# Kernel optimization log

Measured on AMD Instinct MI355X. Metric: run time of the kernel, lower is better.

Reference implementation:

```python
import jax, jax.numpy as jnp
import numpy as np
from jax import lax

N, H, W, CIN = 64, 256, 256, 3   # batch, image HxW, RGB
C, K = 32, 5                     # cross-conv channels / kernel size (from reshape(-1,32,5,5))
ADIM, AHID = 4, 256              # action dim, action-encoder hidden


def _conv(x, w, b, stride, pad):
    # x [N,C,H,W], w [O,I,kh,kw] (torch OIHW cross-correlation semantics)
    y = lax.conv_general_dilated(x, w, (stride, stride), [(pad, pad), (pad, pad)],
                                 dimension_numbers=('NCHW', 'OIHW', 'NCHW'))
    return y + b[None, :, None, None]


def cross_convolve(feat, kernels):
    # feat [N,C,h,w], kernels [N,C,K,K]; per-sample per-channel 'same' conv (padding=2).
    # Equivalent to the original N*C loop of tiny F.conv2d calls: one depthwise
    # (grouped, feature_group_count=C) conv per sample, vmapped over the batch.
    def one(x, k):  # x [C,h,w], k [C,K,K]
        y = lax.conv_general_dilated(x[None], k[:, None], (1, 1), [(2, 2), (2, 2)],
                                     dimension_numbers=('NCHW', 'OIHW', 'NCHW'),
                                     feature_group_count=C)
        return y[0]
    return jax.vmap(one)(feat, kernels)


def setup_inputs() -> dict:
    key = jax.random.key(0)
    ks = jax.random.split(key, 10)
    g = lambda i, shape, s: jax.random.normal(ks[i], shape, jnp.float32) * s
    return {
        'images': jax.random.normal(ks[0], (N, H, W, CIN), jnp.float32),
        'actions': jax.random.normal(ks[1], (N, ADIM), jnp.float32),
        # phys_encoder: conv(3->32,k5,s2,p2) relu, conv(32->32,k5,s2,p2) relu
        'pe_w1': g(2, (C, CIN, 5, 5), 0.08), 'pe_b1': jnp.zeros((C,), jnp.float32),
        'pe_w2': g(3, (C, C, 5, 5), 0.04), 'pe_b2': jnp.zeros((C,), jnp.float32),
        # action_encoder MLP: ADIM -> AHID -> C*K*K (=800)
        'ae_w1': g(4, (ADIM, AHID), 0.3), 'ae_b1': jnp.zeros((AHID,), jnp.float32),
        'ae_w2': g(5, (AHID, C * K * K), 0.05), 'ae_b2': jnp.zeros((C * K * K,), jnp.float32),
        # motion_predictor: conv(32->32,k3,p1) relu, conv(32->2,k3,p1)
        'mp_w1': g(6, (C, C, 3, 3), 0.06), 'mp_b1': jnp.zeros((C,), jnp.float32),
        'mp_w2': g(7, (2, C, 3, 3), 0.06), 'mp_b2': jnp.zeros((2,), jnp.float32),
    }


def reference(images, actions, pe_w1, pe_b1, pe_w2, pe_b2,
              ae_w1, ae_b1, ae_w2, ae_b2, mp_w1, mp_b1, mp_w2, mp_b2):
    x = jnp.transpose(images, (0, 3, 1, 2))                 # NHWC -> NCHW
    h = jax.nn.relu(_conv(x, pe_w1, pe_b1, 2, 2))           # [N,32,128,128]
    h = jax.nn.relu(_conv(h, pe_w2, pe_b2, 2, 2))           # [N,32,64,64]
    a = jax.nn.relu(actions @ ae_w1 + ae_b1)
    a = (a @ ae_w2 + ae_b2).reshape(-1, C, K, K)            # per-sample kernels [N,32,5,5]
    sa = cross_convolve(h, a)                               # [N,32,64,64]
    f = jax.nn.relu(_conv(sa, mp_w1, mp_b1, 1, 1))
    flow = _conv(f, mp_w2, mp_b2, 1, 1)                     # [N,2,64,64]
    return flow
```

## Files before the change

kernel.cpp:

```cpp
#include <hip/hip_runtime.h>


typedef __attribute__((ext_vector_type(8))) short bf16x8;
typedef __attribute__((ext_vector_type(4))) float f32x4;
typedef __attribute__((ext_vector_type(16))) float f32x16;

__device__ __forceinline__ unsigned short f2bf(float f) {
    unsigned int u = __float_as_uint(f);
    u = (u + 0x7FFFu + ((u >> 16) & 1u)) >> 16;
    return (unsigned short)u;
}
__device__ __forceinline__ float bf2f(unsigned short h) {
    return __uint_as_float(((unsigned int)h) << 16);
}

__global__ __launch_bounds__(64) void zero_border_kernel(unsigned int* t, int R, int pad) {
    int row = blockIdx.x % R;
    int n   = blockIdx.x / R;
    int tid = threadIdx.x;
    unsigned int* rp = t + (size_t)(n * R + row) * R * 16;
    if (row < pad || row >= R - pad) {
        for (int i = tid; i < R * 16; i += 64) rp[i] = 0u;
    } else {
        for (int i = tid; i < pad * 16; i += 64) {
            rp[i] = 0u;
            rp[(size_t)(R - pad) * 16 + i] = 0u;
        }
    }
}

__global__ __launch_bounds__(256) void pad_img_kernel(const float* __restrict__ img,
                                                      unsigned short* __restrict__ imgp) {
    const int py = blockIdx.x % 260;
    const int n  = blockIdx.x / 260;
    const int iy = py - 2;
    const bool rowok = (iy >= 0) && (iy < 256);
    const float* srow = img + ((size_t)n * 256 + (rowok ? iy : 0)) * 768;
    unsigned short* drow = imgp + (size_t)(n * 260 + py) * 1056;
    for (int s = threadIdx.x; s < 1056; s += 256) {
        int px = s >> 2, c = s & 3;
        int ix = px - 2;
        float v = 0.f;
        if (rowok && c < 3 && ix >= 0 && ix < 256) v = srow[ix * 3 + c];
        drow[s] = f2bf(v);
    }
}

__global__ __launch_bounds__(256) void repack_conv1b(const float* __restrict__ src, unsigned short* __restrict__ dst) {
    int idx = blockIdx.x * 256 + threadIdx.x;
    if (idx >= 5120) return;
    int kh = idx / 1024, r = idx % 1024, o = r / 32, k = r % 32, dx = k >> 2, c = k & 3;
    float v = (dx < 5 && c < 3) ? src[o * 75 + c * 25 + kh * 5 + dx] : 0.f;
    dst[idx] = f2bf(v);
}
__global__ __launch_bounds__(256) void repack_conv2(const float* __restrict__ src, unsigned short* __restrict__ dst) {
    int idx = blockIdx.x * 256 + threadIdx.x;
    if (idx >= 25600) return;
    int co = idx / 800, r = idx % 800, ci = r / 25, tap = r % 25;
    dst[(tap * 32 + co) * 32 + ci] = f2bf(src[idx]);
}
__global__ __launch_bounds__(256) void repack_mp1(const float* __restrict__ src, unsigned short* __restrict__ dst) {
    int idx = blockIdx.x * 256 + threadIdx.x;
    if (idx >= 9216) return;
    int co = idx / 288, r = idx % 288, ci = r / 9, tap = r % 9;
    dst[(tap * 32 + co) * 32 + ci] = f2bf(src[idx]);
}
__global__ __launch_bounds__(256) void repack_mp2b(const float* __restrict__ src, unsigned short* __restrict__ dst) {
    int idx = blockIdx.x * 256 + threadIdx.x;
    if (idx >= 4608) return;
    int tap = idx / 512, r = idx % 512, co = r / 32, ci = r % 32;
    float v = (co < 2) ? src[co * 288 + ci * 9 + tap] : 0.f;
    dst[idx] = f2bf(v);
}

__global__ __launch_bounds__(256) void mlp_kernel(const float* __restrict__ actions,
                                                  const float* __restrict__ w1,
                                                  const float* __restrict__ b1,
                                                  const float* __restrict__ w2,
                                                  const float* __restrict__ b2,
                                                  float* __restrict__ aout) {
    int n = blockIdx.y;
    int t = threadIdx.x;
    __shared__ float hid[256];
    float a0 = actions[n * 4 + 0], a1 = actions[n * 4 + 1];
    float a2 = actions[n * 4 + 2], a3 = actions[n * 4 + 3];
    float acc = b1[t];
    acc += a0 * w1[0 * 256 + t] + a1 * w1[1 * 256 + t] +
           a2 * w1[2 * 256 + t] + a3 * w1[3 * 256 + t];
    hid[t] = fmaxf(acc, 0.0f);
    __syncthreads();
    int o = blockIdx.x * 200 + t;
    if (t < 200) {
        float s = b2[o];
        #pragma unroll 4
        for (int i = 0; i < 256; ++i) s += hid[i] * w2[i * 800 + o];
        aout[n * 800 + o] = s;
    }
}

__global__ __launch_bounds__(256) void conv1_mfma(const unsigned short* __restrict__ imgp,
                                                  const short* __restrict__ B1,
                                                  const float* __restrict__ bias,
                                                  unsigned short* __restrict__ h1p) {
    const int tid = threadIdx.x;
    const int lane = tid & 63;
    const int w = tid >> 6;
    const int n = blockIdx.y;
    const int cohalf = w & 1;
    const int oy = blockIdx.x * 2 + (w >> 1);
    const int ml = lane & 15;
    const int kg = lane >> 4;

    bf16x8 bfrag[5];
    #pragma unroll
    for (int kh = 0; kh < 5; ++kh)
        bfrag[kh] = *(const bf16x8*)(B1 + ((kh * 32 + cohalf * 16 + ml) * 32 + kg * 8));
    const float bia = bias[cohalf * 16 + ml];
    const int co = cohalf * 16 + ml;

    f32x4 acc[8];
    #pragma unroll
    for (int t = 0; t < 8; ++t) acc[t] = (f32x4){bia, bia, bia, bia};

    #pragma unroll
    for (int kh = 0; kh < 5; ++kh) {
        const unsigned short* rowbase = imgp + (size_t)(n * 260 + 2 * oy + kh) * 1056;
        #pragma unroll
        for (int t = 0; t < 8; ++t) {
            const int px0 = 2 * (16 * t + ml) + 2 * kg;
            bf16x8 af = *(const bf16x8*)(rowbase + px0 * 4);
            acc[t] = __builtin_amdgcn_mfma_f32_16x16x32_bf16(af, bfrag[kh], acc[t], 0, 0, 0);
        }
    }
    #pragma unroll
    for (int t = 0; t < 8; ++t) {
        #pragma unroll
        for (int r = 0; r < 4; ++r) {
            const int px = 16 * t + kg * 4 + r;
            h1p[((size_t)(n * 132 + oy + 2) * 132 + px + 2) * 32 + co] = f2bf(fmaxf(acc[t][r], 0.f));
        }
    }
}

__global__ __launch_bounds__(256, 6) void conv2_mfma32(const unsigned short* __restrict__ h1p,
                                                       const unsigned int* __restrict__ B,
                                                       const float* __restrict__ bias,
                                                       unsigned short* __restrict__ h2p) {
    __shared__ unsigned int Bs[5 * 32 * 20];
    const int tid = threadIdx.x;
    const int lane = tid & 63;
    const int w = tid >> 6;
    const int n = blockIdx.y;
    const int oy = blockIdx.x * 2 + (w >> 1);
    const int x0 = (w & 1) * 32;
    const int co = lane & 31;
    const int kgrp = lane >> 5;

    const float bia = bias[co];
    f32x16 acc;
    #pragma unroll
    for (int r = 0; r < 16; ++r) acc[r] = bia;

    const unsigned short* bbase = (const unsigned short*)Bs + co * 40 + kgrp * 8;
    const int px0 = 2 * (x0 + co);

    for (int kh = 0; kh < 5; ++kh) {
        if (kh) __syncthreads();
        const unsigned int* src = B + kh * 2560;
        #pragma unroll
        for (int i = tid; i < 2560; i += 256) {
            int row = i >> 4, p = i & 15;
            Bs[row * 20 + p] = src[i];
        }
        __syncthreads();

        const unsigned short* rowbase = h1p + (size_t)(n * 132 + 2 * oy + kh) * (132 * 32) + kgrp * 8;
        #pragma unroll
        for (int kw = 0; kw < 5; ++kw) {
            bf16x8 a0 = *(const bf16x8*)(rowbase + (px0 + kw) * 32);
            bf16x8 a1 = *(const bf16x8*)(rowbase + (px0 + kw) * 32 + 16);
            bf16x8 b0 = *(const bf16x8*)(bbase + kw * (32 * 40));
            bf16x8 b1 = *(const bf16x8*)(bbase + kw * (32 * 40) + 16);
            acc = __builtin_amdgcn_mfma_f32_32x32x16_bf16(a0, b0, acc, 0, 0, 0);
            acc = __builtin_amdgcn_mfma_f32_32x32x16_bf16(a1, b1, acc, 0, 0, 0);
        }
    }
    #pragma unroll
    for (int r = 0; r < 16; ++r) {
        const int px = (r & 3) + 8 * (r >> 2) + 4 * kgrp;
        const int ox = x0 + px;
        h2p[((size_t)(n * 68 + oy + 2) * 68 + ox + 2) * 32 + co] = f2bf(fmaxf(acc[r], 0.f));
    }
}

__global__ __launch_bounds__(256) void xconv_kernel(const unsigned short* __restrict__ h2p,
                                                    const float* __restrict__ ker,
                                                    unsigned short* __restrict__ sap) {
    __shared__ __align__(16) unsigned short tile[12 * 68 * 32];
    const int tid = threadIdx.x;
    const int n = blockIdx.x;
    const int rb = blockIdx.y;
    const unsigned short* src = h2p + (size_t)(n * 68 + rb * 8) * (68 * 32);
    for (int i = tid; i < 3264; i += 256)
        *(uint4*)(tile + i * 8) = *(const uint4*)(src + i * 8);
    const int ci = tid & 31, xg = tid >> 5;
    const float* kp = ker + (size_t)(n * 32 + ci) * 25;
    float k[25];
    #pragma unroll
    for (int t = 0; t < 25; ++t) k[t] = kp[t];
    __syncthreads();

    float acc[8][8];
    #pragma unroll
    for (int r = 0; r < 8; ++r)
        #pragma unroll
        for (int j = 0; j < 8; ++j) acc[r][j] = 0.f;

    #pragma unroll
    for (int ir = 0; ir < 12; ++ir) {
        float v[12];
        #pragma unroll
        for (int t = 0; t < 12; ++t)
            v[t] = bf2f(tile[(ir * 68 + xg * 8 + t) * 32 + ci]);
        #pragma unroll
        for (int kh = 0; kh < 5; ++kh) {
            const int r = ir - kh;
            if (r >= 0 && r < 8) {
                #pragma unroll
                for (int j = 0; j < 8; ++j) {
                    float s = acc[r][j];
                    #pragma unroll
                    for (int kw = 0; kw < 5; ++kw) s += k[kh * 5 + kw] * v[j + kw];
                    acc[r][j] = s;
                }
            }
        }
    }
    #pragma unroll
    for (int r = 0; r < 8; ++r)
        #pragma unroll
        for (int j = 0; j < 8; ++j)
            sap[((size_t)(n * 66 + rb * 8 + r + 1) * 66 + xg * 8 + j + 1) * 32 + ci] = f2bf(acc[r][j]);
}

__global__ __launch_bounds__(256, 6) void mp1_mfma32(const unsigned short* __restrict__ sap,
                                                     const unsigned int* __restrict__ B,
                                                     const float* __restrict__ bias,
                                                     unsigned short* __restrict__ fp) {
    __shared__ unsigned int Bs[9 * 32 * 20];
    const int tid = threadIdx.x;
    #pragma unroll
    for (int i = tid; i < 4608; i += 256) {
        int row = i >> 4, p = i & 15;
        Bs[row * 20 + p] = B[i];
    }
    __syncthreads();

    const int lane = tid & 63;
    const int w = tid >> 6;
    const int n = blockIdx.y;
    const int oy = blockIdx.x * 2 + (w >> 1);
    const int x0 = (w & 1) * 32;
    const int co = lane & 31;
    const int kgrp = lane >> 5;

    const float bia = bias[co];
    f32x16 acc;
    #pragma unroll
    for (int r = 0; r < 16; ++r) acc[r] = bia;

    const unsigned short* bbase = (const unsigned short*)Bs + co * 40 + kgrp * 8;
    const int px0 = x0 + co;

    #pragma unroll
    for (int kh = 0; kh < 3; ++kh) {
        const unsigned short* rowbase = sap + (size_t)(n * 66 + oy + kh) * (66 * 32) + kgrp * 8;
        #pragma unroll
        for (int kw = 0; kw < 3; ++kw) {
            const int tap = kh * 3 + kw;
            bf16x8 a0 = *(const bf16x8*)(rowbase + (px0 + kw) * 32);
            bf16x8 a1 = *(const bf16x8*)(rowbase + (px0 + kw) * 32 + 16);
            bf16x8 b0 = *(const bf16x8*)(bbase + tap * (32 * 40));
            bf16x8 b1 = *(const bf16x8*)(bbase + tap * (32 * 40) + 16);
            acc = __builtin_amdgcn_mfma_f32_32x32x16_bf16(a0, b0, acc, 0, 0, 0);
            acc = __builtin_amdgcn_mfma_f32_32x32x16_bf16(a1, b1, acc, 0, 0, 0);
        }
    }
    #pragma unroll
    for (int r = 0; r < 16; ++r) {
        const int px = (r & 3) + 8 * (r >> 2) + 4 * kgrp;
        const int ox = x0 + px;
        fp[((size_t)(n * 66 + oy + 1) * 66 + ox + 1) * 32 + co] = f2bf(fmaxf(acc[r], 0.f));
    }
}

__global__ __launch_bounds__(256) void mp2_mfma(const unsigned short* __restrict__ fpb,
                                                const short* __restrict__ B,
                                                const float* __restrict__ bias,
                                                float* __restrict__ out) {
    const int tid = threadIdx.x;
    const int lane = tid & 63;
    const int w = tid >> 6;
    const int n = blockIdx.y;
    const int oy = blockIdx.x * 4 + w;
    const int ml = lane & 15;
    const int kg = lane >> 4;

    bf16x8 bfrag[9];
    #pragma unroll
    for (int t = 0; t < 9; ++t)
        bfrag[t] = *(const bf16x8*)(B + ((t * 16 + ml) * 32 + kg * 8));
    const float bia = (ml < 2) ? bias[ml] : 0.f;

    f32x4 acc[4];
    #pragma unroll
    for (int t = 0; t < 4; ++t) acc[t] = (f32x4){bia, bia, bia, bia};

    #pragma unroll
    for (int kh = 0; kh < 3; ++kh) {
        const unsigned short* rowbase = fpb + (size_t)(n * 66 + oy + kh) * (66 * 32);
        #pragma unroll
        for (int kw = 0; kw < 3; ++kw) {
            #pragma unroll
            for (int t = 0; t < 4; ++t) {
                bf16x8 af = *(const bf16x8*)(rowbase + (16 * t + ml + kw) * 32 + kg * 8);
                acc[t] = __builtin_amdgcn_mfma_f32_16x16x32_bf16(af, bfrag[kh * 3 + kw], acc[t], 0, 0, 0);
            }
        }
    }
    if (ml < 2) {
        #pragma unroll
        for (int t = 0; t < 4; ++t) {
            #pragma unroll
            for (int r = 0; r < 4; ++r) {
                const int px = 16 * t + kg * 4 + r;
                out[(size_t)n * 8192 + (size_t)ml * 4096 + (size_t)oy * 64 + px] = acc[t][r];
            }
        }
    }
}

extern "C" void kernel_launch(void* const* d_in, const int* in_sizes, int n_in,
                              void* d_out, int out_size, void* d_ws, size_t ws_size,
                              hipStream_t stream) {
    (void)in_sizes; (void)n_in; (void)out_size; (void)ws_size;
    const float* images  = (const float*)d_in[0];
    const float* actions = (const float*)d_in[1];
    const float* pe_w1   = (const float*)d_in[2];
    const float* pe_b1   = (const float*)d_in[3];
    const float* pe_w2   = (const float*)d_in[4];
    const float* pe_b2   = (const float*)d_in[5];
    const float* ae_w1   = (const float*)d_in[6];
    const float* ae_b1   = (const float*)d_in[7];
    const float* ae_w2   = (const float*)d_in[8];
    const float* ae_b2   = (const float*)d_in[9];
    const float* mp_w1   = (const float*)d_in[10];
    const float* mp_b1   = (const float*)d_in[11];
    const float* mp_w2   = (const float*)d_in[12];
    const float* mp_b2   = (const float*)d_in[13];
    float* out = (float*)d_out;

    char* ws = (char*)d_ws;
    float* a_ker          = (float*)(ws + 0);
    unsigned short* B1    = (unsigned short*)(ws + 204800);
    unsigned short* B2    = (unsigned short*)(ws + 215040);
    unsigned short* Bm1   = (unsigned short*)(ws + 266240);
    unsigned short* Bm2   = (unsigned short*)(ws + 284672);
    unsigned short* h1p   = (unsigned short*)(ws + 524288);
    unsigned short* imgp  = (unsigned short*)(ws + 71892992);
    unsigned short* h2p   = (unsigned short*)(ws + 71892992);
    unsigned short* sap   = (unsigned short*)(ws + 90832896);
    unsigned short* fpb   = (unsigned short*)(ws + 108675072);

    repack_conv1b<<<20, 256, 0, stream>>>(pe_w1, B1);
    repack_conv2<<<100, 256, 0, stream>>>(pe_w2, B2);
    repack_mp1<<<36, 256, 0, stream>>>(mp_w1, Bm1);
    repack_mp2b<<<18, 256, 0, stream>>>(mp_w2, Bm2);
    mlp_kernel<<<dim3(4, 64), 256, 0, stream>>>(actions, ae_w1, ae_b1, ae_w2, ae_b2, a_ker);

    zero_border_kernel<<<64 * 132, 64, 0, stream>>>((unsigned int*)h1p, 132, 2);
    zero_border_kernel<<<64 * 66, 64, 0, stream>>>((unsigned int*)fpb, 66, 1);

    pad_img_kernel<<<64 * 260, 256, 0, stream>>>(images, imgp);
    conv1_mfma<<<dim3(64, 64), 256, 0, stream>>>(imgp, (const short*)B1, pe_b1, h1p);

    zero_border_kernel<<<64 * 68, 64, 0, stream>>>((unsigned int*)h2p, 68, 2);
    zero_border_kernel<<<64 * 66, 64, 0, stream>>>((unsigned int*)sap, 66, 1);

    conv2_mfma32<<<dim3(32, 64), 256, 0, stream>>>(h1p, (const unsigned int*)B2, pe_b2, h2p);
    xconv_kernel<<<dim3(64, 8), 256, 0, stream>>>(h2p, a_ker, sap);
    mp1_mfma32<<<dim3(32, 64), 256, 0, stream>>>(sap, (const unsigned int*)Bm1, mp_b1, fpb);
    mp2_mfma<<<dim3(16, 64), 256, 0, stream>>>(fpb, (const short*)Bm2, mp_b2, out);
}
```

Baseline: 296.1 us.

## Merge repack and border-zero launches, batch loads before MFMAs, retune launch bounds

Folds the four weight-repack kernels into one launch and merges pairs of border-zeroing launches into single two-slice grids, cutting the number of kernel launches. In the conv1, conv2, mp1 and mp2 kernels, all A/B fragment loads for a kernel row are issued into register arrays before the MFMA chain, so memory latency can overlap. It also changes the occupancy hints in the launch bounds, which trades register budget against waves per SIMD.

```diff
diff --git a/kernel.cpp b/kernel.cpp
--- a/kernel.cpp
+++ b/kernel.cpp
@@ -14,10 +14,15 @@
     return __uint_as_float(((unsigned int)h) << 16);
 }
 
-__global__ __launch_bounds__(64) void zero_border_kernel(unsigned int* t, int R, int pad) {
-    int row = blockIdx.x % R;
-    int n   = blockIdx.x / R;
-    int tid = threadIdx.x;
+__global__ __launch_bounds__(64) void zero_border2(unsigned int* t0, int R0, int p0,
+                                                   unsigned int* t1, int R1, int p1) {
+    unsigned int* t = blockIdx.y ? t1 : t0;
+    const int R = blockIdx.y ? R1 : R0;
+    const int pad = blockIdx.y ? p1 : p0;
+    const int row = blockIdx.x % R;
+    const int n = blockIdx.x / R;
+    if (n >= 64) return;
+    const int tid = threadIdx.x;
     unsigned int* rp = t + (size_t)(n * R + row) * R * 16;
     if (row < pad || row >= R - pad) {
         for (int i = tid; i < R * 16; i += 64) rp[i] = 0u;
@@ -46,31 +51,33 @@
     }
 }
 
-__global__ __launch_bounds__(256) void repack_conv1b(const float* __restrict__ src, unsigned short* __restrict__ dst) {
+__global__ __launch_bounds__(256) void repack_all(const float* __restrict__ pe_w1,
+                                                  const float* __restrict__ pe_w2,
+                                                  const float* __restrict__ mp_w1,
+                                                  const float* __restrict__ mp_w2,
+                                                  unsigned short* __restrict__ B1,
+                                                  unsigned short* __restrict__ B2,
+                                                  unsigned short* __restrict__ Bm1,
+                                                  unsigned short* __restrict__ Bm2) {
     int idx = blockIdx.x * 256 + threadIdx.x;
-    if (idx >= 5120) return;
-    int kh = idx / 1024, r = idx % 1024, o = r / 32, k = r % 32, dx = k >> 2, c = k & 3;
-    float v = (dx < 5 && c < 3) ? src[o * 75 + c * 25 + kh * 5 + dx] : 0.f;
-    dst[idx] = f2bf(v);
-}
-__global__ __launch_bounds__(256) void repack_conv2(const float* __restrict__ src, unsigned short* __restrict__ dst) {
-    int idx = blockIdx.x * 256 + threadIdx.x;
-    if (idx >= 25600) return;
-    int co = idx / 800, r = idx % 800, ci = r / 25, tap = r % 25;
-    dst[(tap * 32 + co) * 32 + ci] = f2bf(src[idx]);
-}
-__global__ __launch_bounds__(256) void repack_mp1(const float* __restrict__ src, unsigned short* __restrict__ dst) {
-    int idx = blockIdx.x * 256 + threadIdx.x;
-    if (idx >= 9216) return;
-    int co = idx / 288, r = idx % 288, ci = r / 9, tap = r % 9;
-    dst[(tap * 32 + co) * 32 + ci] = f2bf(src[idx]);
-}
-__global__ __launch_bounds__(256) void repack_mp2b(const float* __restrict__ src, unsigned short* __restrict__ dst) {
-    int idx = blockIdx.x * 256 + threadIdx.x;
-    if (idx >= 4608) return;
-    int tap = idx / 512, r = idx % 512, co = r / 32, ci = r % 32;
-    float v = (co < 2) ? src[co * 288 + ci * 9 + tap] : 0.f;
-    dst[idx] = f2bf(v);
+    if (idx < 5120) {
+        int kh = idx / 1024, r = idx % 1024, o = r / 32, k = r % 32, dx = k >> 2, c = k & 3;
+        float v = (dx < 5 && c < 3) ? pe_w1[o * 75 + c * 25 + kh * 5 + dx] : 0.f;
+        B1[idx] = f2bf(v);
+    } else if (idx < 30720) {
+        int i = idx - 5120;
+        int co = i / 800, r = i % 800, ci = r / 25, tap = r % 25;
+        B2[(tap * 32 + co) * 32 + ci] = f2bf(pe_w2[i]);
+    } else if (idx < 39936) {
+        int i = idx - 30720;
+        int co = i / 288, r = i % 288, ci = r / 9, tap = r % 9;
+        Bm1[(tap * 32 + co) * 32 + ci] = f2bf(mp_w1[i]);
+    } else if (idx < 44544) {
+        int i = idx - 39936;
+        int tap = i / 512, r = i % 512, co = r / 32, ci = r % 32;
+        float v = (co < 2) ? mp_w2[co * 288 + ci * 9 + tap] : 0.f;
+        Bm2[i] = f2bf(v);
+    }
 }
 
 __global__ __launch_bounds__(256) void mlp_kernel(const float* __restrict__ actions,
@@ -98,10 +105,10 @@
     }
 }
 
-__global__ __launch_bounds__(256) void conv1_mfma(const unsigned short* __restrict__ imgp,
-                                                  const short* __restrict__ B1,
-                                                  const float* __restrict__ bias,
-                                                  unsigned short* __restrict__ h1p) {
+__global__ __launch_bounds__(256, 4) void conv1_mfma(const unsigned short* __restrict__ imgp,
+                                                     const short* __restrict__ B1,
+                                                     const float* __restrict__ bias,
+                                                     unsigned short* __restrict__ h1p) {
     const int tid = threadIdx.x;
     const int lane = tid & 63;
     const int w = tid >> 6;
@@ -122,15 +129,17 @@
     #pragma unroll
     for (int t = 0; t < 8; ++t) acc[t] = (f32x4){bia, bia, bia, bia};
 
-    #pragma unroll
     for (int kh = 0; kh < 5; ++kh) {
         const unsigned short* rowbase = imgp + (size_t)(n * 260 + 2 * oy + kh) * 1056;
+        bf16x8 af[8];
         #pragma unroll
         for (int t = 0; t < 8; ++t) {
             const int px0 = 2 * (16 * t + ml) + 2 * kg;
-            bf16x8 af = *(const bf16x8*)(rowbase + px0 * 4);
-            acc[t] = __builtin_amdgcn_mfma_f32_16x16x32_bf16(af, bfrag[kh], acc[t], 0, 0, 0);
-        }
+            af[t] = *(const bf16x8*)(rowbase + px0 * 4);
+        }
+        #pragma unroll
+        for (int t = 0; t < 8; ++t)
+            acc[t] = __builtin_amdgcn_mfma_f32_16x16x32_bf16(af[t], bfrag[kh], acc[t], 0, 0, 0);
     }
     #pragma unroll
     for (int t = 0; t < 8; ++t) {
@@ -142,7 +151,7 @@
     }
 }
 
-__global__ __launch_bounds__(256, 6) void conv2_mfma32(const unsigned short* __restrict__ h1p,
+__global__ __launch_bounds__(256, 4) void conv2_mfma32(const unsigned short* __restrict__ h1p,
                                                        const unsigned int* __restrict__ B,
                                                        const float* __restrict__ bias,
                                                        unsigned short* __restrict__ h2p) {
@@ -175,14 +184,18 @@
         __syncthreads();
 
         const unsigned short* rowbase = h1p + (size_t)(n * 132 + 2 * oy + kh) * (132 * 32) + kgrp * 8;
+        bf16x8 a[10], b[10];
         #pragma unroll
         for (int kw = 0; kw < 5; ++kw) {
-            bf16x8 a0 = *(const bf16x8*)(rowbase + (px0 + kw) * 32);
-            bf16x8 a1 = *(const bf16x8*)(rowbase + (px0 + kw) * 32 + 16);
-            bf16x8 b0 = *(const bf16x8*)(bbase + kw * (32 * 40));
-            bf16x8 b1 = *(const bf16x8*)(bbase + kw * (32 * 40) + 16);
-            acc = __builtin_amdgcn_mfma_f32_32x32x16_bf16(a0, b0, acc, 0, 0, 0);
-            acc = __builtin_amdgcn_mfma_f32_32x32x16_bf16(a1, b1, acc, 0, 0, 0);
+            a[2 * kw]     = *(const bf16x8*)(rowbase + (px0 + kw) * 32);
+            a[2 * kw + 1] = *(const bf16x8*)(rowbase + (px0 + kw) * 32 + 16);
+            b[2 * kw]     = *(const bf16x8*)(bbase + kw * (32 * 40));
+            b[2 * kw + 1] = *(const bf16x8*)(bbase + kw * (32 * 40) + 16);
+        }
+        #pragma unroll
+        for (int kw = 0; kw < 5; ++kw) {
+            acc = __builtin_amdgcn_mfma_f32_32x32x16_bf16(a[2 * kw], b[2 * kw], acc, 0, 0, 0);
+            acc = __builtin_amdgcn_mfma_f32_32x32x16_bf16(a[2 * kw + 1], b[2 * kw + 1], acc, 0, 0, 0);
         }
     }
     #pragma unroll
@@ -243,7 +256,7 @@
             sap[((size_t)(n * 66 + rb * 8 + r + 1) * 66 + xg * 8 + j + 1) * 32 + ci] = f2bf(acc[r][j]);
 }
 
-__global__ __launch_bounds__(256, 6) void mp1_mfma32(const unsigned short* __restrict__ sap,
+__global__ __launch_bounds__(256, 5) void mp1_mfma32(const unsigned short* __restrict__ sap,
                                                      const unsigned int* __restrict__ B,
                                                      const float* __restrict__ bias,
                                                      unsigned short* __restrict__ fp) {
@@ -272,18 +285,21 @@
     const unsigned short* bbase = (const unsigned short*)Bs + co * 40 + kgrp * 8;
     const int px0 = x0 + co;
 
-    #pragma unroll
     for (int kh = 0; kh < 3; ++kh) {
         const unsigned short* rowbase = sap + (size_t)(n * 66 + oy + kh) * (66 * 32) + kgrp * 8;
+        bf16x8 a[6], b[6];
         #pragma unroll
         for (int kw = 0; kw < 3; ++kw) {
             const int tap = kh * 3 + kw;
-            bf16x8 a0 = *(const bf16x8*)(rowbase + (px0 + kw) * 32);
-            bf16x8 a1 = *(const bf16x8*)(rowbase + (px0 + kw) * 32 + 16);
-            bf16x8 b0 = *(const bf16x8*)(bbase + tap * (32 * 40));
-            bf16x8 b1 = *(const bf16x8*)(bbase + tap * (32 * 40) + 16);
-            acc = __builtin_amdgcn_mfma_f32_32x32x16_bf16(a0, b0, acc, 0, 0, 0);
-            acc = __builtin_amdgcn_mfma_f32_32x32x16_bf16(a1, b1, acc, 0, 0, 0);
+            a[2 * kw]     = *(const bf16x8*)(rowbase + (px0 + kw) * 32);
+            a[2 * kw + 1] = *(const bf16x8*)(rowbase + (px0 + kw) * 32 + 16);
+            b[2 * kw]     = *(const bf16x8*)(bbase + tap * (32 * 40));
+            b[2 * kw + 1] = *(const bf16x8*)(bbase + tap * (32 * 40) + 16);
+        }
+        #pragma unroll
+        for (int kw = 0; kw < 3; ++kw) {
+            acc = __builtin_amdgcn_mfma_f32_32x32x16_bf16(a[2 * kw], b[2 * kw], acc, 0, 0, 0);
+            acc = __builtin_amdgcn_mfma_f32_32x32x16_bf16(a[2 * kw + 1], b[2 * kw + 1], acc, 0, 0, 0);
         }
     }
     #pragma unroll
@@ -294,10 +310,10 @@
     }
 }
 
-__global__ __launch_bounds__(256) void mp2_mfma(const unsigned short* __restrict__ fpb,
-                                                const short* __restrict__ B,
-                                                const float* __restrict__ bias,
-                                                float* __restrict__ out) {
+__global__ __launch_bounds__(256, 4) void mp2_mfma(const unsigned short* __restrict__ fpb,
+                                                   const short* __restrict__ B,
+                                                   const float* __restrict__ bias,
+                                                   float* __restrict__ out) {
     const int tid = threadIdx.x;
     const int lane = tid & 63;
     const int w = tid >> 6;
@@ -316,17 +332,19 @@
     #pragma unroll
     for (int t = 0; t < 4; ++t) acc[t] = (f32x4){bia, bia, bia, bia};
 
-    #pragma unroll
     for (int kh = 0; kh < 3; ++kh) {
         const unsigned short* rowbase = fpb + (size_t)(n * 66 + oy + kh) * (66 * 32);
-        #pragma unroll
-        for (int kw = 0; kw < 3; ++kw) {
+        bf16x8 af[12];
+        #pragma unroll
+        for (int kw = 0; kw < 3; ++kw)
             #pragma unroll
-            for (int t = 0; t < 4; ++t) {
-                bf16x8 af = *(const bf16x8*)(rowbase + (16 * t + ml + kw) * 32 + kg * 8);
-                acc[t] = __builtin_amdgcn_mfma_f32_16x16x32_bf16(af, bfrag[kh * 3 + kw], acc[t], 0, 0, 0);
-            }
-        }
+            for (int t = 0; t < 4; ++t)
+                af[kw * 4 + t] = *(const bf16x8*)(rowbase + (16 * t + ml + kw) * 32 + kg * 8);
+        #pragma unroll
+        for (int kw = 0; kw < 3; ++kw)
+            #pragma unroll
+            for (int t = 0; t < 4; ++t)
+                acc[t] = __builtin_amdgcn_mfma_f32_16x16x32_bf16(af[kw * 4 + t], bfrag[kh * 3 + kw], acc[t], 0, 0, 0);
     }
     if (ml < 2) {
         #pragma unroll
@@ -372,20 +390,16 @@
     unsigned short* sap   = (unsigned short*)(ws + 90832896);
     unsigned short* fpb   = (unsigned short*)(ws + 108675072);
 
-    repack_conv1b<<<20, 256, 0, stream>>>(pe_w1, B1);
-    repack_conv2<<<100, 256, 0, stream>>>(pe_w2, B2);
-    repack_mp1<<<36, 256, 0, stream>>>(mp_w1, Bm1);
-    repack_mp2b<<<18, 256, 0, stream>>>(mp_w2, Bm2);
+    repack_all<<<174, 256, 0, stream>>>(pe_w1, pe_w2, mp_w1, mp_w2, B1, B2, Bm1, Bm2);
     mlp_kernel<<<dim3(4, 64), 256, 0, stream>>>(actions, ae_w1, ae_b1, ae_w2, ae_b2, a_ker);
-
-    zero_border_kernel<<<64 * 132, 64, 0, stream>>>((unsigned int*)h1p, 132, 2);
-    zero_border_kernel<<<64 * 66, 64, 0, stream>>>((unsigned int*)fpb, 66, 1);
+    zero_border2<<<dim3(64 * 132, 2), 64, 0, stream>>>((unsigned int*)h1p, 132, 2,
+                                                       (unsigned int*)fpb, 66, 1);
 
     pad_img_kernel<<<64 * 260, 256, 0, stream>>>(images, imgp);
     conv1_mfma<<<dim3(64, 64), 256, 0, stream>>>(imgp, (const short*)B1, pe_b1, h1p);
 
-    zero_border_kernel<<<64 * 68, 64, 0, stream>>>((unsigned int*)h2p, 68, 2);
-    zero_border_kernel<<<64 * 66, 64, 0, stream>>>((unsigned int*)sap, 66, 1);
+    zero_border2<<<dim3(64 * 68, 2), 64, 0, stream>>>((unsigned int*)h2p, 68, 2,
+                                                      (unsigned int*)sap, 66, 1);
 
     conv2_mfma32<<<dim3(32, 64), 256, 0, stream>>>(h1p, (const unsigned int*)B2, pe_b2, h2p);
     xconv_kernel<<<dim3(64, 8), 256, 0, stream>>>(h2p, a_ker, sap);
```

Result: faster. 288.0 us (-2.7%).
